# Kernel tuning notes

Measured on AMD Instinct MI355X. Metric: run time of the kernel, lower is better.

Reference implementation:

```python
import jax, jax.numpy as jnp
import numpy as np

NUM_HEAD = 8
DIM_HEAD = 32
IN_DIM = 256  # = NUM_HEAD * DIM_HEAD
SLEN = 1024
BSZ = 8


def setup_inputs() -> dict:
    key = jax.random.key(0)
    ks = jax.random.split(key, 6)
    std = 1.0 / np.sqrt(DIM_HEAD).astype(np.float32)
    h = jax.random.normal(ks[0], (SLEN, BSZ, IN_DIM), dtype=jnp.float32)
    W_y = std * jax.random.normal(ks[1], (1, NUM_HEAD, DIM_HEAD, DIM_HEAD), dtype=jnp.float32)
    W_q = std * jax.random.normal(ks[2], (1, NUM_HEAD, DIM_HEAD, DIM_HEAD), dtype=jnp.float32)
    W_k = std * jax.random.normal(ks[3], (1, NUM_HEAD, DIM_HEAD, DIM_HEAD), dtype=jnp.float32)
    w_b = std * jax.random.normal(ks[4], (1, NUM_HEAD, DIM_HEAD, 4), dtype=jnp.float32)
    # out_linear: Linear(H*d -> in_dim, bias=False); torch weight shape (in_dim, H*d)
    W_out = jax.random.normal(ks[5], (IN_DIM, NUM_HEAD * DIM_HEAD), dtype=jnp.float32) / np.sqrt(NUM_HEAD * DIM_HEAD).astype(np.float32)
    return {"h": h, "W_y": W_y, "W_q": W_q, "W_k": W_k, "w_b": w_b, "W_out": W_out}


def _read(W, v):
    # W: (B,H,d,d), v: (B,H,d) -> (B,H,d)
    return jnp.einsum('bhij,bhj->bhi', W, v)


def _read_b(wb, v):
    # wb: (B,H,d,4), v: (B,H,d) -> (B,H,4)
    return jnp.einsum('bhik,bhi->bhk', wb, v)


def _srwm_forward(h, W_y, W_q, W_k, w_b, W_out):
    slen, bsz, _ = h.shape
    # reshape to heads and softmax the input (as in the torch forward)
    x = jax.nn.softmax(h.reshape(slen, bsz, NUM_HEAD, DIM_HEAD), axis=-1)  # (S,B,H,d)
    bc = lambda W: jnp.broadcast_to(W, (bsz,) + W.shape[1:])
    carry0 = (bc(W_y), bc(W_q), bc(W_k), bc(w_b))

    def step(carry, xt):
        Wy, Wq, Wk, wb = carry  # (B,H,d,d) x3, (B,H,d,4)
        yt = _read(Wy, xt)                                   # output read with current Wy
        qt = jax.nn.softmax(_read(Wq, xt), axis=-1)          # query
        kt = jax.nn.softmax(_read(Wk, xt), axis=-1)          # key
        bt = jax.nn.sigmoid(_read_b(wb, xt))                 # (B,H,4) learning rates
        # delta-rule self-referential update: W += beta * (W q - W k) (x) k
        dy = _read(Wy, qt) - _read(Wy, kt)
        dq = _read(Wq, qt) - _read(Wq, kt)
        dk = _read(Wk, qt) - _read(Wk, kt)
        db = _read_b(wb, qt) - _read_b(wb, kt)               # (B,H,4)
        outer = lambda u: u[..., :, None] * kt[..., None, :]
        Wy = Wy + bt[..., 0][..., None, None] * outer(dy)
        Wq = Wq + bt[..., 1][..., None, None] * outer(dq)
        Wk = Wk + bt[..., 2][..., None, None] * outer(dk)
        wb = wb + bt[..., 3][..., None, None] * (kt[..., :, None] * db[..., None, :])
        return (Wy, Wq, Wk, wb), yt

    _, ys = jax.lax.scan(step, carry0, x)                    # ys: (S,B,H,d)
    out = ys.reshape(slen, bsz, NUM_HEAD * DIM_HEAD) @ W_out.T  # (S,B,in_dim)
    return h + out  # dropout p=0 -> identity; residual


def reference(h, W_y, W_q, W_k, w_b, W_out):
    return _srwm_forward(h, W_y, W_q, W_k, w_b, W_out)
```

## Files before the change

### kernel.cpp

```cpp
#include <hip/hip_runtime.h>

#define DEV __device__ __forceinline__


template <int CTRL>
DEV float dppf(float x) {
  return __int_as_float(__builtin_amdgcn_update_dpp(
      0, __float_as_int(x), CTRL, 0xF, 0xF, true));
}

DEV float wsum32(float v) {
  v += dppf<0xB1>(v);
  v += dppf<0x4E>(v);
  v += dppf<0x141>(v);
  v += dppf<0x140>(v);
#if __has_builtin(__builtin_amdgcn_permlane16_swap)
  {
    auto p = __builtin_amdgcn_permlane16_swap(
        __float_as_uint(v), __float_as_uint(v), false, false);
    v = __uint_as_float(p[0]) + __uint_as_float(p[1]);
  }
#else
  v += __shfl_xor(v, 16, 64);
#endif
  return v;
}

DEV float halfsum(float v) {
#if __has_builtin(__builtin_amdgcn_permlane32_swap)
  auto p = __builtin_amdgcn_permlane32_swap(
      __float_as_uint(v), __float_as_uint(v), false, false);
  return __uint_as_float(p[0]) + __uint_as_float(p[1]);
#else
  return v + __shfl_xor(v, 32, 64);
#endif
}

#define SLEN 1024
#define NH 8
#define DH 32
#define HSTRIDE 2048


__global__ __launch_bounds__(256)
void srwm_xsm(const float* __restrict__ h, float* __restrict__ x) {
  int i = blockIdx.x * 256 + threadIdx.x;
  float e = __expf(h[i]);
  x[i] = __fdividef(e, wsum32(e));
}


#define DSR128(dst, addr, off) \
  asm volatile("ds_read_b128 %0, %1 offset:%2" : "=&v"(dst) : "v"(addr), "i"(off))
#define DSR32(dst, addr, off) \
  asm volatile("ds_read_b32 %0, %1 offset:%2" : "=&v"(dst) : "v"(addr), "i"(off))

#define REGION(T, P, QV, KV, BW, QN, KN, BN, XS, XP)                          \
  {                                                                           \
                 \
    asm volatile("s_waitcnt lgkmcnt(0)");                                     \
    __builtin_amdgcn_sched_barrier(0);                                        \
                         \
    float d0=0.f,d1=0.f,d2=0.f,d3=0.f,s0=0.f,s1=0.f,s2=0.f,s3=0.f;            \
    _Pragma("unroll") for (int i = 0; i < 4; ++i) {                           \
      float4 qv = QV[i], kv = KV[i], xv = XS[i];                              \
      d0 = fmaf(W[4*i+0], qv.x - kv.x, d0);                                   \
      d1 = fmaf(W[4*i+1], qv.y - kv.y, d1);                                   \
      d2 = fmaf(W[4*i+2], qv.z - kv.z, d2);                                   \
      d3 = fmaf(W[4*i+3], qv.w - kv.w, d3);                                   \
      s0 = fmaf(kv.x, xv.x, s0);                                              \
      s1 = fmaf(kv.y, xv.y, s1);                                              \
      s2 = fmaf(kv.z, xv.z, s2);                                              \
      s3 = fmaf(kv.w, xv.w, s3);                                              \
    }                                                                         \
    float dsum = halfsum((d0 + d1) + (d2 + d3));                              \
    float sv   = halfsum((s0 + s1) + (s2 + s3));                              \
    float u  = BW * dsum;                                                     \
    float aA = fmaf(u, sv, preA);                                             \
    if (w == 0) {                                                             \
      if (lane < DH) xb[(size_t)(T) * HSTRIDE + lane] = aA;          \
    } else if (w == 1) {                                                      \
      float e = __expf(aA); shb[(P)*72 + r] = __fdividef(e, wsum32(e));       \
    } else if (w == 2) {                                                      \
      float e = __expf(aA); shb[(P)*72 + 32 + r] = __fdividef(e, wsum32(e));  \
    } else {                                                                  \
      float sg = __fdividef(1.f, 1.f + __expf(-aA));                          \
      if (lane < 4) shb[(P)*72 + 64 + lane] = sg;                             \
    }                                                                         \
    __builtin_amdgcn_sched_barrier(0);                                        \
    asm volatile("s_waitcnt lgkmcnt(0)");                                     \
    __builtin_amdgcn_sched_barrier(0);                                        \
    __builtin_amdgcn_s_barrier();                                             \
    __builtin_amdgcn_sched_barrier(0);                                        \
             \
    DSR128(QN[0], adC, (P)*288 +   0);                                        \
    DSR128(QN[1], adC, (P)*288 +  16);                                        \
    DSR128(QN[2], adC, (P)*288 +  32);                                        \
    DSR128(QN[3], adC, (P)*288 +  48);                                        \
    DSR128(KN[0], adC, (P)*288 + 128);                                        \
    DSR128(KN[1], adC, (P)*288 + 144);                                        \
    DSR128(KN[2], adC, (P)*288 + 160);                                        \
    DSR128(KN[3], adC, (P)*288 + 176);                                        \
    DSR32 (BN,    adB, (P)*288 + 256);                                        \
    __builtin_amdgcn_sched_barrier(0);                                        \
        \
    _Pragma("unroll") for (int i = 0; i < 4; ++i) {                           \
      float4 kv = KV[i];                                                      \
      W[4*i+0] = fmaf(u, kv.x, W[4*i+0]);                                     \
      W[4*i+1] = fmaf(u, kv.y, W[4*i+1]);                                     \
      W[4*i+2] = fmaf(u, kv.z, W[4*i+2]);                                     \
      W[4*i+3] = fmaf(u, kv.w, W[4*i+3]);                                     \
    }                                                                         \
    int t2 = (T) + 2; if (t2 > SLEN - 1) t2 = SLEN - 1;                       \
    { const float* xp_ = xb + (size_t)t2 * HSTRIDE + c0;                      \
      _Pragma("unroll") for (int i = 0; i < 4; ++i)                           \
        XS[i] = *(const float4*)(xp_ + 4 * i); }                              \
    float p0=0.f,p1=0.f,p2=0.f,p3=0.f;                                        \
    _Pragma("unroll") for (int i = 0; i < 4; ++i) {                           \
      float4 xv = XP[i];                                                      \
      p0 = fmaf(W[4*i+0], xv.x, p0);                                          \
      p1 = fmaf(W[4*i+1], xv.y, p1);                                          \
      p2 = fmaf(W[4*i+2], xv.z, p2);                                          \
      p3 = fmaf(W[4*i+3], xv.w, p3);                                          \
    }                                                                         \
    preA = halfsum((p0 + p1) + (p2 + p3));                                    \
  }

__global__ __launch_bounds__(256, 1)
void srwm_scan(const float* __restrict__ Wy0, const float* __restrict__ Wq0,
               const float* __restrict__ Wk0, const float* __restrict__ wb0,
               float* xy) {
  __shared__ float shb[2 * 72];

  const int bh   = blockIdx.x;
  const int hd   = bh & 7;
  const int w    = threadIdx.x >> 6;
  const int lane = threadIdx.x & 63;
  const int r    = lane & 31;
  const int c0   = (lane >> 5) * 16;

  const uint32_t lbase = (uint32_t)(uintptr_t)&shb[0];
  const uint32_t adC   = lbase + c0 * 4;
  const uint32_t adB   = lbase + w * 4;

  float W[16];
  if (w < 3) {
    const float* src = (w == 0) ? Wy0 : (w == 1) ? Wq0 : Wk0;
    const float* p = src + (hd * DH + r) * DH + c0;
#pragma unroll
    for (int j = 0; j < 16; j += 4) *(float4*)&W[j] = *(const float4*)(p + j);
  } else {
    const int kk = r & 3;
#pragma unroll
    for (int j = 0; j < 16; ++j) W[j] = wb0[(hd * DH + c0 + j) * 4 + kk];
  }

  float* xb = xy + bh * DH;

  float4 X0[4], X1[4];
#pragma unroll
  for (int i = 0; i < 4; ++i) {
    X0[i] = *(const float4*)(xb + c0 + 4 * i);
    X1[i] = *(const float4*)(xb + HSTRIDE + c0 + 4 * i);
  }
  float p0 = 0.f, p1 = 0.f, p2 = 0.f, p3 = 0.f;
#pragma unroll
  for (int i = 0; i < 4; ++i) {
    float4 xv = X0[i];
    p0 = fmaf(W[4*i+0], xv.x, p0);
    p1 = fmaf(W[4*i+1], xv.y, p1);
    p2 = fmaf(W[4*i+2], xv.z, p2);
    p3 = fmaf(W[4*i+3], xv.w, p3);
  }
  float preA = halfsum((p0 + p1) + (p2 + p3));

  float4 QA[4], KA[4], QB[4], KB[4];
  const float4 z4 = {0.f, 0.f, 0.f, 0.f};
#pragma unroll
  for (int i = 0; i < 4; ++i) { QA[i] = z4; KA[i] = z4; }
  float BwA = 0.f, BwB = 0.f;

  __syncthreads();

  for (int t = 0; t < SLEN; t += 2) {
    REGION(t,     0, QA, KA, BwA, QB, KB, BwB, X0, X1);
    REGION(t + 1, 1, QB, KB, BwB, QA, KA, BwA, X1, X0);
  }
}


__global__ __launch_bounds__(256)
void srwm_proj(const float* __restrict__ h, const float* __restrict__ ys,
               const float* __restrict__ Wout, float* __restrict__ out) {
  __shared__ float ytile[32][256];
  const int r0  = blockIdx.x * 32;
  const int tid = threadIdx.x;

  const float4* src = (const float4*)(ys + (size_t)r0 * 256);
  float4*       dst = (float4*)(&ytile[0][0]);
#pragma unroll
  for (int i = 0; i < 8; ++i) dst[tid + i * 256] = src[tid + i * 256];
  __syncthreads();

  float acc[32];
#pragma unroll
  for (int m = 0; m < 32; ++m) acc[m] = 0.f;

  const float* wrow = Wout + (size_t)tid * 256;
  for (int k = 0; k < 256; k += 4) {
    float4 wv = *(const float4*)(wrow + k);
#pragma unroll
    for (int m = 0; m < 32; ++m) {
      float4 y4 = *(const float4*)(&ytile[m][k]);
      acc[m] = fmaf(wv.x, y4.x,
               fmaf(wv.y, y4.y,
               fmaf(wv.z, y4.z,
               fmaf(wv.w, y4.w, acc[m]))));
    }
  }

#pragma unroll
  for (int m = 0; m < 32; ++m) {
    int row = r0 + m;
    out[(size_t)row * 256 + tid] = h[(size_t)row * 256 + tid] + acc[m];
  }
}


extern "C" void kernel_launch(void* const* d_in, const int* in_sizes, int n_in,
                              void* d_out, int out_size, void* d_ws, size_t ws_size,
                              hipStream_t stream) {
  const float* h    = (const float*)d_in[0];
  const float* Wy0  = (const float*)d_in[1];
  const float* Wq0  = (const float*)d_in[2];
  const float* Wk0  = (const float*)d_in[3];
  const float* wb0  = (const float*)d_in[4];
  const float* Wout = (const float*)d_in[5];
  float* out = (float*)d_out;

  srwm_xsm <<<SLEN * HSTRIDE / 256, 256, 0, stream>>>(h, out);
  srwm_scan<<<64, 256, 0, stream>>>(Wy0, Wq0, Wk0, wb0, out);
  srwm_proj<<<256, 256, 0, stream>>>(h, out, Wout, out);
}
```

Before: 591.5 us.

## Defer softmax normalization of q/k into consumer reductions to shorten critical path

The producer warps for q and k now write unnormalized exponentials to shared memory instead of performing a wave-wide sum and divide before the barrier. Consumers compute the sums of the exponentials alongside the dot products and scale by reciprocals afterwards, which removes a cross-lane reduction from the serial per-timestep chain. The cost is more FMAs and two extra half-wave reductions per step in every consumer, plus possible numerical differences because the exponentials are not max-subtracted. The initial q/k buffers are set to ones so the first-step sums are nonzero and the reciprocals stay finite.

```diff
diff --git a/kernel.cpp b/kernel.cpp
--- a/kernel.cpp
+++ b/kernel.cpp
@@ -55,34 +55,50 @@
 #define DSR32(dst, addr, off) \
   asm volatile("ds_read_b32 %0, %1 offset:%2" : "=&v"(dst) : "v"(addr), "i"(off))
 
-#define REGION(T, P, QV, KV, BW, QN, KN, BN, XS, XP)                          \
+#define REGION(T, P, EQ, EK, BW, EQN, EKN, BN, XS, XP)                        \
   {                                                                           \
                  \
     asm volatile("s_waitcnt lgkmcnt(0)");                                     \
     __builtin_amdgcn_sched_barrier(0);                                        \
-                         \
-    float d0=0.f,d1=0.f,d2=0.f,d3=0.f,s0=0.f,s1=0.f,s2=0.f,s3=0.f;            \
+                       \
+    float aq0=0.f,aq1=0.f,aq2=0.f,aq3=0.f;                                    \
+    float ak0=0.f,ak1=0.f,ak2=0.f,ak3=0.f;                                    \
+    float ex0=0.f,ex1=0.f,ex2=0.f,ex3=0.f;                                    \
+    float psq0=0.f,psq1=0.f,psk0=0.f,psk1=0.f;                                \
     _Pragma("unroll") for (int i = 0; i < 4; ++i) {                           \
-      float4 qv = QV[i], kv = KV[i], xv = XS[i];                              \
-      d0 = fmaf(W[4*i+0], qv.x - kv.x, d0);                                   \
-      d1 = fmaf(W[4*i+1], qv.y - kv.y, d1);                                   \
-      d2 = fmaf(W[4*i+2], qv.z - kv.z, d2);                                   \
-      d3 = fmaf(W[4*i+3], qv.w - kv.w, d3);                                   \
-      s0 = fmaf(kv.x, xv.x, s0);                                              \
-      s1 = fmaf(kv.y, xv.y, s1);                                              \
-      s2 = fmaf(kv.z, xv.z, s2);                                              \
-      s3 = fmaf(kv.w, xv.w, s3);                                              \
-    }                                                                         \
-    float dsum = halfsum((d0 + d1) + (d2 + d3));                              \
-    float sv   = halfsum((s0 + s1) + (s2 + s3));                              \
-    float u  = BW * dsum;                                                     \
-    float aA = fmaf(u, sv, preA);                                             \
+      float4 qv = EQ[i], kv = EK[i], xv = XS[i];                              \
+      aq0 = fmaf(W[4*i+0], qv.x, aq0);                                        \
+      aq1 = fmaf(W[4*i+1], qv.y, aq1);                                        \
+      aq2 = fmaf(W[4*i+2], qv.z, aq2);                                        \
+      aq3 = fmaf(W[4*i+3], qv.w, aq3);                                        \
+      ak0 = fmaf(W[4*i+0], kv.x, ak0);                                        \
+      ak1 = fmaf(W[4*i+1], kv.y, ak1);                                        \
+      ak2 = fmaf(W[4*i+2], kv.z, ak2);                                        \
+      ak3 = fmaf(W[4*i+3], kv.w, ak3);                                        \
+      ex0 = fmaf(kv.x, xv.x, ex0);                                            \
+      ex1 = fmaf(kv.y, xv.y, ex1);                                            \
+      ex2 = fmaf(kv.z, xv.z, ex2);                                            \
+      ex3 = fmaf(kv.w, xv.w, ex3);                                            \
+      psq0 += (qv.x + qv.y); psq1 += (qv.z + qv.w);                           \
+      psk0 += (kv.x + kv.y); psk1 += (kv.z + kv.w);                           \
+    }                                                                         \
+    float Sq = halfsum(psq0 + psq1);                                          \
+    float Sk = halfsum(psk0 + psk1);                                          \
+    float rq = __fdividef(1.f, Sq);                                           \
+    float rk = __fdividef(1.f, Sk);                                           \
+    float pd = rq * ((aq0 + aq1) + (aq2 + aq3))                               \
+             - rk * ((ak0 + ak1) + (ak2 + ak3));                              \
+    float d_   = halfsum(pd);                                                 \
+    float ekx  = halfsum((ex0 + ex1) + (ex2 + ex3));                          \
+    float ukr  = BW * d_ * rk;                                                \
+    float aA   = fmaf(ukr, ekx, preA);                                        \
+        \
     if (w == 0) {                                                             \
       if (lane < DH) xb[(size_t)(T) * HSTRIDE + lane] = aA;          \
     } else if (w == 1) {                                                      \
-      float e = __expf(aA); shb[(P)*72 + r] = __fdividef(e, wsum32(e));       \
+      shb[(P)*72 + r] = __expf(aA);                                           \
     } else if (w == 2) {                                                      \
-      float e = __expf(aA); shb[(P)*72 + 32 + r] = __fdividef(e, wsum32(e));  \
+      shb[(P)*72 + 32 + r] = __expf(aA);                                      \
     } else {                                                                  \
       float sg = __fdividef(1.f, 1.f + __expf(-aA));                          \
       if (lane < 4) shb[(P)*72 + 64 + lane] = sg;                             \
@@ -93,23 +109,23 @@
     __builtin_amdgcn_s_barrier();                                             \
     __builtin_amdgcn_sched_barrier(0);                                        \
              \
-    DSR128(QN[0], adC, (P)*288 +   0);                                        \
-    DSR128(QN[1], adC, (P)*288 +  16);                                        \
-    DSR128(QN[2], adC, (P)*288 +  32);                                        \
-    DSR128(QN[3], adC, (P)*288 +  48);                                        \
-    DSR128(KN[0], adC, (P)*288 + 128);                                        \
-    DSR128(KN[1], adC, (P)*288 + 144);                                        \
-    DSR128(KN[2], adC, (P)*288 + 160);                                        \
-    DSR128(KN[3], adC, (P)*288 + 176);                                        \
+    DSR128(EQN[0], adC, (P)*288 +   0);                                       \
+    DSR128(EQN[1], adC, (P)*288 +  16);                                       \
+    DSR128(EQN[2], adC, (P)*288 +  32);                                       \
+    DSR128(EQN[3], adC, (P)*288 +  48);                                       \
+    DSR128(EKN[0], adC, (P)*288 + 128);                                       \
+    DSR128(EKN[1], adC, (P)*288 + 144);                                       \
+    DSR128(EKN[2], adC, (P)*288 + 160);                                       \
+    DSR128(EKN[3], adC, (P)*288 + 176);                                       \
     DSR32 (BN,    adB, (P)*288 + 256);                                        \
     __builtin_amdgcn_sched_barrier(0);                                        \
-        \
+       \
     _Pragma("unroll") for (int i = 0; i < 4; ++i) {                           \
-      float4 kv = KV[i];                                                      \
-      W[4*i+0] = fmaf(u, kv.x, W[4*i+0]);                                     \
-      W[4*i+1] = fmaf(u, kv.y, W[4*i+1]);                                     \
-      W[4*i+2] = fmaf(u, kv.z, W[4*i+2]);                                     \
-      W[4*i+3] = fmaf(u, kv.w, W[4*i+3]);                                     \
+      float4 kv = EK[i];                                                      \
+      W[4*i+0] = fmaf(ukr, kv.x, W[4*i+0]);                                   \
+      W[4*i+1] = fmaf(ukr, kv.y, W[4*i+1]);                                   \
+      W[4*i+2] = fmaf(ukr, kv.z, W[4*i+2]);                                   \
+      W[4*i+3] = fmaf(ukr, kv.w, W[4*i+3]);                                   \
     }                                                                         \
     int t2 = (T) + 2; if (t2 > SLEN - 1) t2 = SLEN - 1;                       \
     { const float* xp_ = xb + (size_t)t2 * HSTRIDE + c0;                      \
@@ -175,9 +191,9 @@
   float preA = halfsum((p0 + p1) + (p2 + p3));
 
   float4 QA[4], KA[4], QB[4], KB[4];
-  const float4 z4 = {0.f, 0.f, 0.f, 0.f};
-#pragma unroll
-  for (int i = 0; i < 4; ++i) { QA[i] = z4; KA[i] = z4; }
+  const float4 one4 = {1.f, 1.f, 1.f, 1.f};
+#pragma unroll
+  for (int i = 0; i < 4; ++i) { QA[i] = one4; KA[i] = one4; }
   float BwA = 0.f, BwB = 0.f;
 
   __syncthreads();
```

After: 685.4 us. +15.9%, slower.

## Interleave two batch-head scans per block to share barriers and hide latency

Applied to the files above, without the earlier changes.

Each scan block now processes two independent (batch, head) recurrences at once, halving the grid from 64 to 32 blocks. The two chains' pre-barrier compute, LDS reads and post-barrier updates are interleaved so one barrier and one LDS wait cover both. This is meant to fill the serial-latency gaps of the per-timestep recurrence with independent work. In exchange it doubles register use per thread and leaves half as many blocks running on the GPU.

```diff
diff --git a/kernel.cpp b/kernel.cpp
--- a/kernel.cpp
+++ b/kernel.cpp
@@ -55,12 +55,8 @@
 #define DSR32(dst, addr, off) \
   asm volatile("ds_read_b32 %0, %1 offset:%2" : "=&v"(dst) : "v"(addr), "i"(off))
 
-#define REGION(T, P, QV, KV, BW, QN, KN, BN, XS, XP)                          \
-  {                                                                           \
-                 \
-    asm volatile("s_waitcnt lgkmcnt(0)");                                     \
-    __builtin_amdgcn_sched_barrier(0);                                        \
-                         \
+#define PRE(T, P, C, QV, KV, BW, XS, PREA, W, XB, UOUT)                       \
+  {                                                                           \
     float d0=0.f,d1=0.f,d2=0.f,d3=0.f,s0=0.f,s1=0.f,s2=0.f,s3=0.f;            \
     _Pragma("unroll") for (int i = 0; i < 4; ++i) {                           \
       float4 qv = QV[i], kv = KV[i], xv = XS[i];                              \
@@ -75,44 +71,46 @@
     }                                                                         \
     float dsum = halfsum((d0 + d1) + (d2 + d3));                              \
     float sv   = halfsum((s0 + s1) + (s2 + s3));                              \
-    float u  = BW * dsum;                                                     \
-    float aA = fmaf(u, sv, preA);                                             \
+    UOUT = BW * dsum;                                                         \
+    float aA = fmaf(UOUT, sv, PREA);                                          \
     if (w == 0) {                                                             \
-      if (lane < DH) xb[(size_t)(T) * HSTRIDE + lane] = aA;          \
+      if (lane < DH) XB[(size_t)(T) * HSTRIDE + lane] = aA;          \
     } else if (w == 1) {                                                      \
-      float e = __expf(aA); shb[(P)*72 + r] = __fdividef(e, wsum32(e));       \
+      float e = __expf(aA);                                                   \
+      shb[(P)*144 + (C)*72 + r] = __fdividef(e, wsum32(e));                   \
     } else if (w == 2) {                                                      \
-      float e = __expf(aA); shb[(P)*72 + 32 + r] = __fdividef(e, wsum32(e));  \
+      float e = __expf(aA);                                                   \
+      shb[(P)*144 + (C)*72 + 32 + r] = __fdividef(e, wsum32(e));              \
     } else {                                                                  \
       float sg = __fdividef(1.f, 1.f + __expf(-aA));                          \
-      if (lane < 4) shb[(P)*72 + 64 + lane] = sg;                             \
-    }                                                                         \
-    __builtin_amdgcn_sched_barrier(0);                                        \
-    asm volatile("s_waitcnt lgkmcnt(0)");                                     \
-    __builtin_amdgcn_sched_barrier(0);                                        \
-    __builtin_amdgcn_s_barrier();                                             \
-    __builtin_amdgcn_sched_barrier(0);                                        \
-             \
-    DSR128(QN[0], adC, (P)*288 +   0);                                        \
-    DSR128(QN[1], adC, (P)*288 +  16);                                        \
-    DSR128(QN[2], adC, (P)*288 +  32);                                        \
-    DSR128(QN[3], adC, (P)*288 +  48);                                        \
-    DSR128(KN[0], adC, (P)*288 + 128);                                        \
-    DSR128(KN[1], adC, (P)*288 + 144);                                        \
-    DSR128(KN[2], adC, (P)*288 + 160);                                        \
-    DSR128(KN[3], adC, (P)*288 + 176);                                        \
-    DSR32 (BN,    adB, (P)*288 + 256);                                        \
-    __builtin_amdgcn_sched_barrier(0);                                        \
-        \
+      if (lane < 4) shb[(P)*144 + (C)*72 + 64 + lane] = sg;                   \
+    }                                                                         \
+  }
+
+#define RD(P, C, QN, KN, BN)                                                  \
+  {                                                                           \
+    DSR128(QN[0], adC, (P)*576 + (C)*288 +   0);                              \
+    DSR128(QN[1], adC, (P)*576 + (C)*288 +  16);                              \
+    DSR128(QN[2], adC, (P)*576 + (C)*288 +  32);                              \
+    DSR128(QN[3], adC, (P)*576 + (C)*288 +  48);                              \
+    DSR128(KN[0], adC, (P)*576 + (C)*288 + 128);                              \
+    DSR128(KN[1], adC, (P)*576 + (C)*288 + 144);                              \
+    DSR128(KN[2], adC, (P)*576 + (C)*288 + 160);                              \
+    DSR128(KN[3], adC, (P)*576 + (C)*288 + 176);                              \
+    DSR32 (BN,    adB, (P)*576 + (C)*288 + 256);                              \
+  }
+
+#define POST(T, KV, U, XS, XP, PREA, W, XB)                                   \
+  {                                                                           \
     _Pragma("unroll") for (int i = 0; i < 4; ++i) {                           \
       float4 kv = KV[i];                                                      \
-      W[4*i+0] = fmaf(u, kv.x, W[4*i+0]);                                     \
-      W[4*i+1] = fmaf(u, kv.y, W[4*i+1]);                                     \
-      W[4*i+2] = fmaf(u, kv.z, W[4*i+2]);                                     \
-      W[4*i+3] = fmaf(u, kv.w, W[4*i+3]);                                     \
+      W[4*i+0] = fmaf(U, kv.x, W[4*i+0]);                                     \
+      W[4*i+1] = fmaf(U, kv.y, W[4*i+1]);                                     \
+      W[4*i+2] = fmaf(U, kv.z, W[4*i+2]);                                     \
+      W[4*i+3] = fmaf(U, kv.w, W[4*i+3]);                                     \
     }                                                                         \
     int t2 = (T) + 2; if (t2 > SLEN - 1) t2 = SLEN - 1;                       \
-    { const float* xp_ = xb + (size_t)t2 * HSTRIDE + c0;                      \
+    { const float* xp_ = XB + (size_t)t2 * HSTRIDE + c0;                      \
       _Pragma("unroll") for (int i = 0; i < 4; ++i)                           \
         XS[i] = *(const float4*)(xp_ + 4 * i); }                              \
     float p0=0.f,p1=0.f,p2=0.f,p3=0.f;                                        \
@@ -123,68 +121,113 @@
       p2 = fmaf(W[4*i+2], xv.z, p2);                                          \
       p3 = fmaf(W[4*i+3], xv.w, p3);                                          \
     }                                                                         \
-    preA = halfsum((p0 + p1) + (p2 + p3));                                    \
+    PREA = halfsum((p0 + p1) + (p2 + p3));                                    \
+  }
+
+#define REGION2(T, P, Q0, K0, B0, QN0, KN0, BN0, XS0, XP0,                    \
+                      Q1, K1, B1, QN1, KN1, BN1, XS1, XP1)                    \
+  {                                                                           \
+    asm volatile("s_waitcnt lgkmcnt(0)");                                     \
+    __builtin_amdgcn_sched_barrier(0);                                        \
+    float u0_, u1_;                                                           \
+    PRE(T, P, 0, Q0, K0, B0, XS0, preA0, W0, xb0, u0_);                       \
+    PRE(T, P, 1, Q1, K1, B1, XS1, preA1, W1, xb1, u1_);                       \
+    __builtin_amdgcn_sched_barrier(0);                                        \
+    asm volatile("s_waitcnt lgkmcnt(0)");                                     \
+    __builtin_amdgcn_sched_barrier(0);                                        \
+    __builtin_amdgcn_s_barrier();                                             \
+    __builtin_amdgcn_sched_barrier(0);                                        \
+    RD(P, 0, QN0, KN0, BN0);                                                  \
+    RD(P, 1, QN1, KN1, BN1);                                                  \
+    __builtin_amdgcn_sched_barrier(0);                                        \
+    POST(T, K0, u0_, XS0, XP0, preA0, W0, xb0);                               \
+    POST(T, K1, u1_, XS1, XP1, preA1, W1, xb1);                               \
   }
 
 __global__ __launch_bounds__(256, 1)
 void srwm_scan(const float* __restrict__ Wy0, const float* __restrict__ Wq0,
                const float* __restrict__ Wk0, const float* __restrict__ wb0,
                float* xy) {
-  __shared__ float shb[2 * 72];
-
-  const int bh   = blockIdx.x;
-  const int hd   = bh & 7;
+  __shared__ float shb[2 * 144];
+
   const int w    = threadIdx.x >> 6;
   const int lane = threadIdx.x & 63;
   const int r    = lane & 31;
   const int c0   = (lane >> 5) * 16;
 
+  const int bh0 = blockIdx.x * 2;
+  const int bh1 = bh0 + 1;
+  const int hd0 = bh0 & 7, hd1 = bh1 & 7;
+
   const uint32_t lbase = (uint32_t)(uintptr_t)&shb[0];
   const uint32_t adC   = lbase + c0 * 4;
   const uint32_t adB   = lbase + w * 4;
 
-  float W[16];
+  float W0[16], W1[16];
   if (w < 3) {
     const float* src = (w == 0) ? Wy0 : (w == 1) ? Wq0 : Wk0;
-    const float* p = src + (hd * DH + r) * DH + c0;
-#pragma unroll
-    for (int j = 0; j < 16; j += 4) *(float4*)&W[j] = *(const float4*)(p + j);
+    const float* p0_ = src + (hd0 * DH + r) * DH + c0;
+    const float* p1_ = src + (hd1 * DH + r) * DH + c0;
+#pragma unroll
+    for (int j = 0; j < 16; j += 4) {
+      *(float4*)&W0[j] = *(const float4*)(p0_ + j);
+      *(float4*)&W1[j] = *(const float4*)(p1_ + j);
+    }
   } else {
     const int kk = r & 3;
 #pragma unroll
-    for (int j = 0; j < 16; ++j) W[j] = wb0[(hd * DH + c0 + j) * 4 + kk];
-  }
-
-  float* xb = xy + bh * DH;
-
-  float4 X0[4], X1[4];
+    for (int j = 0; j < 16; ++j) {
+      W0[j] = wb0[(hd0 * DH + c0 + j) * 4 + kk];
+      W1[j] = wb0[(hd1 * DH + c0 + j) * 4 + kk];
+    }
+  }
+
+  float* xb0 = xy + bh0 * DH;
+  float* xb1 = xy + bh1 * DH;
+
+  float4 XA0[4], XB0[4], XA1[4], XB1[4];
 #pragma unroll
   for (int i = 0; i < 4; ++i) {
-    X0[i] = *(const float4*)(xb + c0 + 4 * i);
-    X1[i] = *(const float4*)(xb + HSTRIDE + c0 + 4 * i);
-  }
-  float p0 = 0.f, p1 = 0.f, p2 = 0.f, p3 = 0.f;
+    XA0[i] = *(const float4*)(xb0 + c0 + 4 * i);
+    XB0[i] = *(const float4*)(xb0 + HSTRIDE + c0 + 4 * i);
+    XA1[i] = *(const float4*)(xb1 + c0 + 4 * i);
+    XB1[i] = *(const float4*)(xb1 + HSTRIDE + c0 + 4 * i);
+  }
+  float preA0, preA1;
+  {
+    float p0=0.f,p1=0.f,p2=0.f,p3=0.f, q0=0.f,q1=0.f,q2=0.f,q3=0.f;
+#pragma unroll
+    for (int i = 0; i < 4; ++i) {
+      float4 xv = XA0[i], yv = XA1[i];
+      p0 = fmaf(W0[4*i+0], xv.x, p0);
+      p1 = fmaf(W0[4*i+1], xv.y, p1);
+      p2 = fmaf(W0[4*i+2], xv.z, p2);
+      p3 = fmaf(W0[4*i+3], xv.w, p3);
+      q0 = fmaf(W1[4*i+0], yv.x, q0);
+      q1 = fmaf(W1[4*i+1], yv.y, q1);
+      q2 = fmaf(W1[4*i+2], yv.z, q2);
+      q3 = fmaf(W1[4*i+3], yv.w, q3);
+    }
+    preA0 = halfsum((p0 + p1) + (p2 + p3));
+    preA1 = halfsum((q0 + q1) + (q2 + q3));
+  }
+
+  float4 QA0[4], KA0[4], QB0[4], KB0[4];
+  float4 QA1[4], KA1[4], QB1[4], KB1[4];
+  const float4 z4 = {0.f, 0.f, 0.f, 0.f};
 #pragma unroll
   for (int i = 0; i < 4; ++i) {
-    float4 xv = X0[i];
-    p0 = fmaf(W[4*i+0], xv.x, p0);
-    p1 = fmaf(W[4*i+1], xv.y, p1);
-    p2 = fmaf(W[4*i+2], xv.z, p2);
-    p3 = fmaf(W[4*i+3], xv.w, p3);
-  }
-  float preA = halfsum((p0 + p1) + (p2 + p3));
-
-  float4 QA[4], KA[4], QB[4], KB[4];
-  const float4 z4 = {0.f, 0.f, 0.f, 0.f};
-#pragma unroll
-  for (int i = 0; i < 4; ++i) { QA[i] = z4; KA[i] = z4; }
-  float BwA = 0.f, BwB = 0.f;
+    QA0[i] = z4; KA0[i] = z4; QA1[i] = z4; KA1[i] = z4;
+  }
+  float BwA0 = 0.f, BwB0 = 0.f, BwA1 = 0.f, BwB1 = 0.f;
 
   __syncthreads();
 
   for (int t = 0; t < SLEN; t += 2) {
-    REGION(t,     0, QA, KA, BwA, QB, KB, BwB, X0, X1);
-    REGION(t + 1, 1, QB, KB, BwB, QA, KA, BwA, X1, X0);
+    REGION2(t,     0, QA0, KA0, BwA0, QB0, KB0, BwB0, XA0, XB0,
+                      QA1, KA1, BwA1, QB1, KB1, BwB1, XA1, XB1);
+    REGION2(t + 1, 1, QB0, KB0, BwB0, QA0, KA0, BwA0, XB0, XA0,
+                      QB1, KB1, BwB1, QA1, KA1, BwA1, XB1, XA1);
   }
 }
 
@@ -239,6 +282,6 @@
   float* out = (float*)d_out;
 
   srwm_xsm <<<SLEN * HSTRIDE / 256, 256, 0, stream>>>(h, out);
-  srwm_scan<<<64, 256, 0, stream>>>(Wy0, Wq0, Wk0, wb0, out);
+  srwm_scan<<<32, 256, 0, stream>>>(Wy0, Wq0, Wk0, wb0, out);
   srwm_proj<<<256, 256, 0, stream>>>(h, out, Wout, out);
 }
```

Result: slower. 1.125 ms (+90.1%).

## Pack two weight matrices per wave in scan kernel, halving block size

Applied to the files above, without the earlier changes.

Each wave of the scan now holds two of the four fast-weight matrices (Wy+Wq, Wk+wb), so the block shrinks from four waves to two. The barrier is cheaper, and the q/k/beta vectors are shared through plain LDS loads instead of inline-asm reads. The loop also strength-reduces the x-prefetch and y-store pointers and peels the final steps to avoid clamping. The trade-off is twice the serial FMA and reduction work per wave on the latency-bound critical path.

```diff
diff --git a/kernel.cpp b/kernel.cpp
--- a/kernel.cpp
+++ b/kernel.cpp
@@ -50,87 +50,96 @@
 }
 
 
-#define DSR128(dst, addr, off) \
-  asm volatile("ds_read_b128 %0, %1 offset:%2" : "=&v"(dst) : "v"(addr), "i"(off))
-#define DSR32(dst, addr, off) \
-  asm volatile("ds_read_b32 %0, %1 offset:%2" : "=&v"(dst) : "v"(addr), "i"(off))
-
-#define REGION(T, P, QV, KV, BW, QN, KN, BN, XS, XP)                          \
+#define BARRIER()                                        \
+  do {                                                   \
+    __builtin_amdgcn_sched_barrier(0);                   \
+    asm volatile("s_waitcnt lgkmcnt(0)");                \
+    __builtin_amdgcn_sched_barrier(0);                   \
+    __builtin_amdgcn_s_barrier();                        \
+    __builtin_amdgcn_sched_barrier(0);                   \
+  } while (0)
+
+#define REGION(P, QV, KV, BP, QN, KN, BPN, XS, XP, XPF, YPTR)                 \
   {                                                                           \
-                 \
-    asm volatile("s_waitcnt lgkmcnt(0)");                                     \
-    __builtin_amdgcn_sched_barrier(0);                                        \
-                         \
-    float d0=0.f,d1=0.f,d2=0.f,d3=0.f,s0=0.f,s1=0.f,s2=0.f,s3=0.f;            \
+                                          \
+    float da0=0.f,da1=0.f,da2=0.f,da3=0.f;                                    \
+    float db0=0.f,db1=0.f,db2=0.f,db3=0.f;                                    \
+    float s0=0.f,s1=0.f,s2=0.f,s3=0.f;                                        \
     _Pragma("unroll") for (int i = 0; i < 4; ++i) {                           \
       float4 qv = QV[i], kv = KV[i], xv = XS[i];                              \
-      d0 = fmaf(W[4*i+0], qv.x - kv.x, d0);                                   \
-      d1 = fmaf(W[4*i+1], qv.y - kv.y, d1);                                   \
-      d2 = fmaf(W[4*i+2], qv.z - kv.z, d2);                                   \
-      d3 = fmaf(W[4*i+3], qv.w - kv.w, d3);                                   \
+      float v0 = qv.x - kv.x, v1 = qv.y - kv.y;                               \
+      float v2 = qv.z - kv.z, v3 = qv.w - kv.w;                               \
+      da0 = fmaf(Wa[4*i+0], v0, da0);                                         \
+      da1 = fmaf(Wa[4*i+1], v1, da1);                                         \
+      da2 = fmaf(Wa[4*i+2], v2, da2);                                         \
+      da3 = fmaf(Wa[4*i+3], v3, da3);                                         \
+      db0 = fmaf(Wb[4*i+0], v0, db0);                                         \
+      db1 = fmaf(Wb[4*i+1], v1, db1);                                         \
+      db2 = fmaf(Wb[4*i+2], v2, db2);                                         \
+      db3 = fmaf(Wb[4*i+3], v3, db3);                                         \
       s0 = fmaf(kv.x, xv.x, s0);                                              \
       s1 = fmaf(kv.y, xv.y, s1);                                              \
       s2 = fmaf(kv.z, xv.z, s2);                                              \
       s3 = fmaf(kv.w, xv.w, s3);                                              \
     }                                                                         \
-    float dsum = halfsum((d0 + d1) + (d2 + d3));                              \
-    float sv   = halfsum((s0 + s1) + (s2 + s3));                              \
-    float u  = BW * dsum;                                                     \
-    float aA = fmaf(u, sv, preA);                                             \
+    float da = halfsum((da0 + da1) + (da2 + da3));                            \
+    float db = halfsum((db0 + db1) + (db2 + db3));                            \
+    float sv = halfsum((s0 + s1) + (s2 + s3));                                \
+    float ua = BP.x * da, ub = BP.y * db;                                     \
+    float aA = fmaf(ua, sv, preAa);                                           \
+    float aB = fmaf(ub, sv, preAb);                                           \
     if (w == 0) {                                                             \
-      if (lane < DH) xb[(size_t)(T) * HSTRIDE + lane] = aA;          \
-    } else if (w == 1) {                                                      \
-      float e = __expf(aA); shb[(P)*72 + r] = __fdividef(e, wsum32(e));       \
-    } else if (w == 2) {                                                      \
-      float e = __expf(aA); shb[(P)*72 + 32 + r] = __fdividef(e, wsum32(e));  \
+      if (lane < DH) *(YPTR) = aA;                                   \
+      float e = __expf(aB);                                                   \
+      shb[(P)*72 + r] = __fdividef(e, wsum32(e));                    \
     } else {                                                                  \
-      float sg = __fdividef(1.f, 1.f + __expf(-aA));                          \
-      if (lane < 4) shb[(P)*72 + 64 + lane] = sg;                             \
-    }                                                                         \
-    __builtin_amdgcn_sched_barrier(0);                                        \
-    asm volatile("s_waitcnt lgkmcnt(0)");                                     \
-    __builtin_amdgcn_sched_barrier(0);                                        \
-    __builtin_amdgcn_s_barrier();                                             \
-    __builtin_amdgcn_sched_barrier(0);                                        \
-             \
-    DSR128(QN[0], adC, (P)*288 +   0);                                        \
-    DSR128(QN[1], adC, (P)*288 +  16);                                        \
-    DSR128(QN[2], adC, (P)*288 +  32);                                        \
-    DSR128(QN[3], adC, (P)*288 +  48);                                        \
-    DSR128(KN[0], adC, (P)*288 + 128);                                        \
-    DSR128(KN[1], adC, (P)*288 + 144);                                        \
-    DSR128(KN[2], adC, (P)*288 + 160);                                        \
-    DSR128(KN[3], adC, (P)*288 + 176);                                        \
-    DSR32 (BN,    adB, (P)*288 + 256);                                        \
-    __builtin_amdgcn_sched_barrier(0);                                        \
-        \
+      float e = __expf(aA);                                                   \
+      shb[(P)*72 + 32 + r] = __fdividef(e, wsum32(e));               \
+      float sg = __fdividef(1.f, 1.f + __expf(-aB));                          \
+      if (lane < 4) shb[(P)*72 + 64 + lane] = sg;                    \
+    }                                                                         \
+    BARRIER();                                                                \
+                                   \
+    _Pragma("unroll") for (int i = 0; i < 4; ++i) {                           \
+      QN[i] = *(const float4*)&shb[(P)*72 + c0 + 4*i];                        \
+      KN[i] = *(const float4*)&shb[(P)*72 + 32 + c0 + 4*i];                   \
+    }                                                                         \
+    BPN = *(const float2*)&shb[(P)*72 + 64 + 2*w];                            \
     _Pragma("unroll") for (int i = 0; i < 4; ++i) {                           \
       float4 kv = KV[i];                                                      \
-      W[4*i+0] = fmaf(u, kv.x, W[4*i+0]);                                     \
-      W[4*i+1] = fmaf(u, kv.y, W[4*i+1]);                                     \
-      W[4*i+2] = fmaf(u, kv.z, W[4*i+2]);                                     \
-      W[4*i+3] = fmaf(u, kv.w, W[4*i+3]);                                     \
-    }                                                                         \
-    int t2 = (T) + 2; if (t2 > SLEN - 1) t2 = SLEN - 1;                       \
-    { const float* xp_ = xb + (size_t)t2 * HSTRIDE + c0;                      \
-      _Pragma("unroll") for (int i = 0; i < 4; ++i)                           \
-        XS[i] = *(const float4*)(xp_ + 4 * i); }                              \
-    float p0=0.f,p1=0.f,p2=0.f,p3=0.f;                                        \
+      Wa[4*i+0] = fmaf(ua, kv.x, Wa[4*i+0]);                                  \
+      Wa[4*i+1] = fmaf(ua, kv.y, Wa[4*i+1]);                                  \
+      Wa[4*i+2] = fmaf(ua, kv.z, Wa[4*i+2]);                                  \
+      Wa[4*i+3] = fmaf(ua, kv.w, Wa[4*i+3]);                                  \
+      Wb[4*i+0] = fmaf(ub, kv.x, Wb[4*i+0]);                                  \
+      Wb[4*i+1] = fmaf(ub, kv.y, Wb[4*i+1]);                                  \
+      Wb[4*i+2] = fmaf(ub, kv.z, Wb[4*i+2]);                                  \
+      Wb[4*i+3] = fmaf(ub, kv.w, Wb[4*i+3]);                                  \
+    }                                                                         \
+    _Pragma("unroll") for (int i = 0; i < 4; ++i)                             \
+      XS[i] = *(const float4*)((XPF) + 4*i);                                  \
+    float pa0=0.f,pa1=0.f,pa2=0.f,pa3=0.f;                                    \
+    float pb0=0.f,pb1=0.f,pb2=0.f,pb3=0.f;                                    \
     _Pragma("unroll") for (int i = 0; i < 4; ++i) {                           \
       float4 xv = XP[i];                                                      \
-      p0 = fmaf(W[4*i+0], xv.x, p0);                                          \
-      p1 = fmaf(W[4*i+1], xv.y, p1);                                          \
-      p2 = fmaf(W[4*i+2], xv.z, p2);                                          \
-      p3 = fmaf(W[4*i+3], xv.w, p3);                                          \
-    }                                                                         \
-    preA = halfsum((p0 + p1) + (p2 + p3));                                    \
-  }
-
-__global__ __launch_bounds__(256, 1)
+      pa0 = fmaf(Wa[4*i+0], xv.x, pa0);                                       \
+      pa1 = fmaf(Wa[4*i+1], xv.y, pa1);                                       \
+      pa2 = fmaf(Wa[4*i+2], xv.z, pa2);                                       \
+      pa3 = fmaf(Wa[4*i+3], xv.w, pa3);                                       \
+      pb0 = fmaf(Wb[4*i+0], xv.x, pb0);                                       \
+      pb1 = fmaf(Wb[4*i+1], xv.y, pb1);                                       \
+      pb2 = fmaf(Wb[4*i+2], xv.z, pb2);                                       \
+      pb3 = fmaf(Wb[4*i+3], xv.w, pb3);                                       \
+    }                                                                         \
+    preAa = halfsum((pa0 + pa1) + (pa2 + pa3));                               \
+    preAb = halfsum((pb0 + pb1) + (pb2 + pb3));                               \
+  }
+
+__global__ __launch_bounds__(128, 1)
 void srwm_scan(const float* __restrict__ Wy0, const float* __restrict__ Wq0,
                const float* __restrict__ Wk0, const float* __restrict__ wb0,
                float* xy) {
-  __shared__ float shb[2 * 72];
+  __align__(16) __shared__ float shb[2 * 72];
 
   const int bh   = blockIdx.x;
   const int hd   = bh & 7;
@@ -139,20 +148,22 @@
   const int r    = lane & 31;
   const int c0   = (lane >> 5) * 16;
 
-  const uint32_t lbase = (uint32_t)(uintptr_t)&shb[0];
-  const uint32_t adC   = lbase + c0 * 4;
-  const uint32_t adB   = lbase + w * 4;
-
-  float W[16];
-  if (w < 3) {
-    const float* src = (w == 0) ? Wy0 : (w == 1) ? Wq0 : Wk0;
-    const float* p = src + (hd * DH + r) * DH + c0;
-#pragma unroll
-    for (int j = 0; j < 16; j += 4) *(float4*)&W[j] = *(const float4*)(p + j);
+  float Wa[16], Wb[16];
+  if (w == 0) {
+    const float* pa = Wy0 + (hd * DH + r) * DH + c0;
+    const float* pb = Wq0 + (hd * DH + r) * DH + c0;
+#pragma unroll
+    for (int j = 0; j < 16; j += 4) {
+      *(float4*)&Wa[j] = *(const float4*)(pa + j);
+      *(float4*)&Wb[j] = *(const float4*)(pb + j);
+    }
   } else {
+    const float* pa = Wk0 + (hd * DH + r) * DH + c0;
+#pragma unroll
+    for (int j = 0; j < 16; j += 4) *(float4*)&Wa[j] = *(const float4*)(pa + j);
     const int kk = r & 3;
 #pragma unroll
-    for (int j = 0; j < 16; ++j) W[j] = wb0[(hd * DH + c0 + j) * 4 + kk];
+    for (int j = 0; j < 16; ++j) Wb[j] = wb0[(hd * DH + c0 + j) * 4 + kk];
   }
 
   float* xb = xy + bh * DH;
@@ -163,28 +174,50 @@
     X0[i] = *(const float4*)(xb + c0 + 4 * i);
     X1[i] = *(const float4*)(xb + HSTRIDE + c0 + 4 * i);
   }
-  float p0 = 0.f, p1 = 0.f, p2 = 0.f, p3 = 0.f;
-#pragma unroll
-  for (int i = 0; i < 4; ++i) {
-    float4 xv = X0[i];
-    p0 = fmaf(W[4*i+0], xv.x, p0);
-    p1 = fmaf(W[4*i+1], xv.y, p1);
-    p2 = fmaf(W[4*i+2], xv.z, p2);
-    p3 = fmaf(W[4*i+3], xv.w, p3);
-  }
-  float preA = halfsum((p0 + p1) + (p2 + p3));
+  float preAa, preAb;
+  {
+    float pa0=0.f,pa1=0.f,pa2=0.f,pa3=0.f;
+    float pb0=0.f,pb1=0.f,pb2=0.f,pb3=0.f;
+#pragma unroll
+    for (int i = 0; i < 4; ++i) {
+      float4 xv = X0[i];
+      pa0 = fmaf(Wa[4*i+0], xv.x, pa0);
+      pa1 = fmaf(Wa[4*i+1], xv.y, pa1);
+      pa2 = fmaf(Wa[4*i+2], xv.z, pa2);
+      pa3 = fmaf(Wa[4*i+3], xv.w, pa3);
+      pb0 = fmaf(Wb[4*i+0], xv.x, pb0);
+      pb1 = fmaf(Wb[4*i+1], xv.y, pb1);
+      pb2 = fmaf(Wb[4*i+2], xv.z, pb2);
+      pb3 = fmaf(Wb[4*i+3], xv.w, pb3);
+    }
+    preAa = halfsum((pa0 + pa1) + (pa2 + pa3));
+    preAb = halfsum((pb0 + pb1) + (pb2 + pb3));
+  }
 
   float4 QA[4], KA[4], QB[4], KB[4];
   const float4 z4 = {0.f, 0.f, 0.f, 0.f};
 #pragma unroll
   for (int i = 0; i < 4; ++i) { QA[i] = z4; KA[i] = z4; }
-  float BwA = 0.f, BwB = 0.f;
+  float2 BPA = {0.f, 0.f}, BPB = {0.f, 0.f};
 
   __syncthreads();
 
-  for (int t = 0; t < SLEN; t += 2) {
-    REGION(t,     0, QA, KA, BwA, QB, KB, BwB, X0, X1);
-    REGION(t + 1, 1, QB, KB, BwB, QA, KA, BwA, X1, X0);
+  const float* xpf = xb + 2 * HSTRIDE + c0;
+  float*       yst = xb + lane;
+
+  for (int t = 0; t < SLEN - 4; t += 2) {
+    REGION(0, QA, KA, BPA, QB, KB, BPB, X0, X1, xpf,           yst);
+    REGION(1, QB, KB, BPB, QA, KA, BPA, X1, X0, xpf + HSTRIDE, yst + HSTRIDE);
+    xpf += 2 * HSTRIDE;
+    yst += 2 * HSTRIDE;
+  }
+  {
+    const float* xlast = xb + (size_t)(SLEN - 1) * HSTRIDE + c0;
+    REGION(0, QA, KA, BPA, QB, KB, BPB, X0, X1, xlast - HSTRIDE, yst);
+    REGION(1, QB, KB, BPB, QA, KA, BPA, X1, X0, xlast,           yst + HSTRIDE);
+    yst += 2 * HSTRIDE;
+    REGION(0, QA, KA, BPA, QB, KB, BPB, X0, X1, xlast, yst);
+    REGION(1, QB, KB, BPB, QA, KA, BPA, X1, X0, xlast, yst + HSTRIDE);
   }
 }
 
@@ -239,6 +272,6 @@
   float* out = (float*)d_out;
 
   srwm_xsm <<<SLEN * HSTRIDE / 256, 256, 0, stream>>>(h, out);
-  srwm_scan<<<64, 256, 0, stream>>>(Wy0, Wq0, Wk0, wb0, out);
+  srwm_scan<<<64, 128, 0, stream>>>(Wy0, Wq0, Wk0, wb0, out);
   srwm_proj<<<256, 256, 0, stream>>>(h, out, Wout, out);
 }
```

Measured after the change: 566.5 us. 4.2% less time.
